# Kernel optimization log

Hardware: AMD Instinct MI355X
Metric: run time of the kernel (lower is better)

## Reference

```python
import jax, jax.numpy as jnp
import numpy as np

EPS = 1e-8


def setup_inputs() -> dict:
    key = jax.random.key(0)
    ks = jax.random.split(key, 10)
    B, Cin, H, W = 16, 256, 64, 64
    D, C = 128, 32
    return {
        "f_curr": jax.random.normal(ks[0], (B, Cin, H, W), jnp.float32),
        "mu_prior": jax.random.normal(ks[1], (B, D, C), jnp.float32),
        "log_sigma_prior": jax.random.normal(ks[2], (B, D, C), jnp.float32),
        "pi_prior": jax.random.uniform(ks[3], (B, C), jnp.float32),
        "mu_post": jax.random.normal(ks[4], (B, D), jnp.float32),
        "log_sigma_post": jax.random.normal(ks[5], (B, D), jnp.float32),
        "noise_cluster": jax.random.normal(ks[6], (B, D), jnp.float32),
        "noise_z": jax.random.normal(ks[7], (B, D), jnp.float32),
        "proj_W": jax.random.normal(ks[8], (Cin, Cin + D), jnp.float32) * 0.02,
        "proj_b": jax.random.normal(ks[9], (Cin,), jnp.float32) * 0.02,
    }


def reference(f_curr, mu_prior, log_sigma_prior, pi_prior, mu_post,
              log_sigma_post, noise_cluster, noise_z, proj_W, proj_b):
    sg = jax.lax.stop_gradient

    # ---- _cluster_sampler (all stats detached in the original) ----
    mu_p, ls_p = sg(mu_post), sg(log_sigma_post)          # [B, D]
    mu_pr, ls_pr = sg(mu_prior), sg(log_sigma_prior)      # [B, D, C]
    z_post = mu_p + jnp.exp(ls_p) * noise_cluster          # Normal(mu, exp(ls)).sample()
    sigma_pr = jnp.exp(ls_pr)
    # Normal log_prob of z_post[:, :, None] under each cluster -> [B, D, C]
    log_probs = (-ls_pr - 0.5 * jnp.log(2.0 * jnp.pi)
                 - (z_post[:, :, None] - mu_pr) ** 2 / (2.0 * sigma_pr ** 2))
    log_prob_c = jnp.sum(log_probs, axis=1)                # [B, C]
    pi_post = jax.nn.softmax(log_prob_c, axis=1)           # [B, C]

    # ---- z_c = Normal(mu_post, exp(ls)+eps).sample()  (no grad: .sample()) ----
    z_c = sg(mu_post + (jnp.exp(log_sigma_post) + EPS) * noise_z)  # [B, D]

    # ---- _f_combine: concat + 1x1 conv, computed as split matmuls ----
    Cin = f_curr.shape[1]
    Wf, Wz = proj_W[:, :Cin], proj_W[:, Cin:]              # [Cin,Cin], [Cin,D]
    bias = jnp.einsum('bd,od->bo', z_c, Wz) + proj_b       # spatially-constant part
    f_out = jnp.einsum('bchw,oc->bohw', f_curr, Wf) + bias[:, :, None, None]

    # ---- _kld ----
    mu_post_e = mu_post[:, :, None]                        # [B, D, 1]
    ls_post_e = log_sigma_post[:, :, None]
    sigma_prior = jnp.exp(log_sigma_prior)
    sigma_post = jnp.exp(ls_post_e)
    kl_g = (log_sigma_prior - ls_post_e
            + (sigma_post ** 2 + (mu_post_e - mu_prior) ** 2)
            / (2.0 * sigma_prior ** 2 + EPS) - 0.5)
    kl_g = jnp.sum(kl_g, axis=1)                           # [B, C]
    kl_g_weighted = jnp.sum(pi_post * kl_g, axis=1)        # [B]
    kl_cat = jnp.sum(pi_post * (jnp.log(pi_post + EPS) - jnp.log(pi_prior + EPS)), axis=1)  # [B]
    kl_std = jnp.sum(-ls_post_e + 0.5 * (jnp.exp(2.0 * ls_post_e) + mu_post_e ** 2) - 0.5,
                     axis=1)                               # [B, 1]
    # NOTE: original torch code broadcasts [B] + [B,1] -> [B,B] before mean; replicated here.
    kld = jnp.mean((kl_g_weighted + kl_cat) + kl_std)

    return f_out, kld
```

## Files before the change

kernel.cpp:

```cpp
#include <hip/hip_runtime.h>
#include <math.h>

#define EPS_F 1e-8f

typedef __attribute__((ext_vector_type(8))) short bf16x8;
typedef __attribute__((ext_vector_type(4))) float f32x4;

__device__ inline short f2bf(float f) {
    union { float f; unsigned u; } v; v.f = f;
    unsigned r = (v.u + 0x7fffu + ((v.u >> 16) & 1u)) >> 16;
    return (short)r;
}

__global__ __launch_bounds__(256) void prelim_kernel(
    const float* __restrict__ mu_prior,
    const float* __restrict__ ls_prior,
    const float* __restrict__ pi_prior,
    const float* __restrict__ mu_post,
    const float* __restrict__ ls_post,
    const float* __restrict__ noise_c,
    const float* __restrict__ noise_z,
    const float* __restrict__ projW,
    const float* __restrict__ projb,
    float* __restrict__ ws_bias,
    short* __restrict__ ws_A,
    float* __restrict__ kld_out)
{
    const int b = blockIdx.x;
    const int t = threadIdx.x;

    {
        const float* wrow = projW + t * 384 + b * 16;
        bf16x8 w0, w1;
#pragma unroll
        for (int j = 0; j < 8; ++j) w0[j] = f2bf(wrow[j]);
#pragma unroll
        for (int j = 0; j < 8; ++j) w1[j] = f2bf(wrow[8 + j]);
        *(bf16x8*)&ws_A[(b * 2 + 0) * 2048 + t * 8] = w0;
        *(bf16x8*)&ws_A[(b * 2 + 1) * 2048 + t * 8] = w1;
    }

    __shared__ float s_zpost[128];
    __shared__ float s_zc[128];
    __shared__ float s_mu[128];
    __shared__ float s_e2[128];
    __shared__ float s_lsp[128];
    __shared__ float s_kstd[128];
    __shared__ float s_p1[8][32];
    __shared__ float s_p2[8][32];

    if (t < 128) {
        const float mu = mu_post[b * 128 + t];
        const float ls = ls_post[b * 128 + t];
        const float el = __expf(ls);
        s_zpost[t] = mu + el * noise_c[b * 128 + t];
        s_zc[t]    = mu + (el + EPS_F) * noise_z[b * 128 + t];
        s_mu[t]    = mu;
        s_e2[t]    = el * el;
        s_lsp[t]   = ls;
        s_kstd[t]  = -ls + 0.5f * (el * el + mu * mu) - 0.5f;
    }
    __syncthreads();

    {
        const int c = t & 31;
        const int g = t >> 5;
        const float* mpB = mu_prior + b * 4096;
        const float* lpB = ls_prior + b * 4096;
        float lp = 0.f, kg = 0.f;
#pragma unroll 4
        for (int j = 0; j < 16; ++j) {
            const int d = g * 16 + j;
            const float mpr  = mpB[d * 32 + c];
            const float lpr  = lpB[d * 32 + c];
            const float inv2 = 0.5f * __expf(-2.f * lpr);
            const float zd   = s_zpost[d] - mpr;
            lp += -lpr - 0.91893853320467274f - zd * zd * inv2;
            const float dm   = s_mu[d] - mpr;
            const float e2pr = __expf(2.f * lpr);
            kg += lpr - s_lsp[d]
                + (s_e2[d] + dm * dm) * __builtin_amdgcn_rcpf(2.f * e2pr + EPS_F)
                - 0.5f;
        }
        s_p1[g][c] = lp;
        s_p2[g][c] = kg;
    }
    __syncthreads();

    if (t < 64) {
        const int c = t & 31;
        float lp = 0.f, kg = 0.f;
#pragma unroll
        for (int g = 0; g < 8; ++g) { lp += s_p1[g][c]; kg += s_p2[g][c]; }
        float ks = s_kstd[c] + s_kstd[c + 32] + s_kstd[c + 64] + s_kstd[c + 96];
        const float pp = pi_prior[b * 32 + c];

        float m = lp;
#pragma unroll
        for (int o = 16; o; o >>= 1) m = fmaxf(m, __shfl_xor(m, o, 32));
        const float e = __expf(lp - m);
        float den = e;
#pragma unroll
        for (int o = 16; o; o >>= 1) den += __shfl_xor(den, o, 32);
        const float pi = e * __builtin_amdgcn_rcpf(den);
        float tot = pi * kg + pi * (__logf(pi + EPS_F) - __logf(pp + EPS_F));
#pragma unroll
        for (int o = 16; o; o >>= 1) tot += __shfl_xor(tot, o, 32);
#pragma unroll
        for (int o = 16; o; o >>= 1) ks += __shfl_xor(ks, o, 32);
        if (t == 0) atomicAdd(kld_out, (tot + ks) * 0.0625f);
    }

    {
        const int o = t;
        const float4* wrow = (const float4*)(projW + o * 384 + 256);
        float sum = projb[o];
#pragma unroll 8
        for (int j = 0; j < 32; ++j) {
            const float4 w = wrow[j];
            sum += s_zc[4 * j + 0] * w.x + s_zc[4 * j + 1] * w.y +
                   s_zc[4 * j + 2] * w.z + s_zc[4 * j + 3] * w.w;
        }
        ws_bias[b * 256 + o] = sum;
    }
}

__global__ __launch_bounds__(256) void gemm_kernel(
    const float* __restrict__ F,
    const short* __restrict__ wsA,
    const float* __restrict__ bias,
    float* __restrict__ O)
{
    const int nT = blockIdx.x;
    const int oT = blockIdx.y;
    const int b  = blockIdx.z;

    __shared__ float s_bias[128];

    const int tid  = threadIdx.x;
    const int lane = tid & 63;
    const int wave = tid >> 6;
    const int wm = wave & 1;
    const int wn = wave >> 1;
    const int kg = lane >> 4;
    const int lm = lane & 15;

    if (tid < 128) s_bias[tid] = bias[b * 256 + oT * 128 + tid];

    const short* aBase = wsA + (size_t)kg * 2048 + (oT * 128 + wm * 64 + lm) * 8;
    const float* bBase = F + (size_t)b * 1048576 + (size_t)(kg * 8) * 4096
                       + nT * 128 + wn * 64 + lm;

    f32x4 acc[4][4];
#pragma unroll
    for (int i = 0; i < 4; ++i)
#pragma unroll
        for (int j = 0; j < 4; ++j) acc[i][j] = (f32x4){0.f, 0.f, 0.f, 0.f};

    float Bbuf[2][32];

#pragma unroll
    for (int nt = 0; nt < 4; ++nt)
#pragma unroll
        for (int j = 0; j < 8; ++j)
            Bbuf[0][nt * 8 + j] = bBase[(size_t)j * 4096 + nt * 16];

#pragma unroll
    for (int kc = 0; kc < 8; ++kc) {
        const int cur = kc & 1, nxt = cur ^ 1;

        if (kc < 7) {
            const float* bp = bBase + (size_t)(kc + 1) * 32 * 4096;
#pragma unroll
            for (int nt = 0; nt < 4; ++nt)
#pragma unroll
                for (int j = 0; j < 8; ++j)
                    Bbuf[nxt][nt * 8 + j] = bp[(size_t)j * 4096 + nt * 16];
        }

        bf16x8 aF[4];
#pragma unroll
        for (int mt = 0; mt < 4; ++mt)
            aF[mt] = *(const bf16x8*)(aBase + (size_t)kc * 8192 + mt * 128);

        bf16x8 bF[4];
#pragma unroll
        for (int nt = 0; nt < 4; ++nt)
#pragma unroll
            for (int j = 0; j < 8; ++j)
                bF[nt][j] = f2bf(Bbuf[cur][nt * 8 + j]);

#pragma unroll
        for (int mt = 0; mt < 4; ++mt)
#pragma unroll
            for (int nt = 0; nt < 4; ++nt)
                acc[mt][nt] = __builtin_amdgcn_mfma_f32_16x16x32_bf16(
                    aF[mt], bF[nt], acc[mt][nt], 0, 0, 0);
    }

    __syncthreads();

    float* Ob = O + (size_t)b * 1048576 + (size_t)oT * 128 * 4096;
    const int rbase = wm * 64 + kg * 4;
    const int cbase = nT * 128 + wn * 64 + lm;
#pragma unroll
    for (int mt = 0; mt < 4; ++mt) {
#pragma unroll
        for (int r = 0; r < 4; ++r) {
            const int row = rbase + mt * 16 + r;
            const float bb = s_bias[row];
            float* orow = Ob + (size_t)row * 4096 + cbase;
#pragma unroll
            for (int nt = 0; nt < 4; ++nt)
                orow[nt * 16] = acc[mt][nt][r] + bb;
        }
    }
}

extern "C" void kernel_launch(void* const* d_in, const int* in_sizes, int n_in,
                              void* d_out, int out_size, void* d_ws, size_t ws_size,
                              hipStream_t stream) {
    const float* f_curr   = (const float*)d_in[0];
    const float* mu_prior = (const float*)d_in[1];
    const float* ls_prior = (const float*)d_in[2];
    const float* pi_prior = (const float*)d_in[3];
    const float* mu_post  = (const float*)d_in[4];
    const float* ls_post  = (const float*)d_in[5];
    const float* noise_c  = (const float*)d_in[6];
    const float* noise_z  = (const float*)d_in[7];
    const float* projW    = (const float*)d_in[8];
    const float* projb    = (const float*)d_in[9];

    float* out = (float*)d_out;
    float* ws  = (float*)d_ws;
    float* ws_bias = ws;
    short* ws_A    = (short*)(ws + 4096);

    float* kld_out = out + 16777216;
    hipMemsetAsync(kld_out, 0, sizeof(float), stream);

    prelim_kernel<<<16, 256, 0, stream>>>(mu_prior, ls_prior, pi_prior, mu_post,
                                          ls_post, noise_c, noise_z, projW, projb,
                                          ws_bias, ws_A, kld_out);
    gemm_kernel<<<dim3(32, 2, 16), 256, 0, stream>>>(f_curr, ws_A, ws_bias, out);
}
```

Before: 164.7 us.

## Stage full-K bf16 F tile in LDS and cover all output channels per block

```diff
diff --git a/kernel.cpp b/kernel.cpp
--- a/kernel.cpp
+++ b/kernel.cpp
@@ -132,24 +132,46 @@
     float* __restrict__ O)
 {
     const int nT = blockIdx.x;
-    const int oT = blockIdx.y;
-    const int b  = blockIdx.z;
-
-    __shared__ float s_bias[128];
+    const int b  = blockIdx.y;
+
+    __shared__ short Bl[32][64][8];
+    __shared__ float s_bias[256];
 
     const int tid  = threadIdx.x;
     const int lane = tid & 63;
     const int wave = tid >> 6;
-    const int wm = wave & 1;
-    const int wn = wave >> 1;
-    const int kg = lane >> 4;
-    const int lm = lane & 15;
-
-    if (tid < 128) s_bias[tid] = bias[b * 256 + oT * 128 + tid];
-
-    const short* aBase = wsA + (size_t)kg * 2048 + (oT * 128 + wm * 64 + lm) * 8;
-    const float* bBase = F + (size_t)b * 1048576 + (size_t)(kg * 8) * 4096
-                       + nT * 128 + wn * 64 + lm;
+    const int kg   = lane >> 4;
+    const int lm   = lane & 15;
+
+    s_bias[tid] = bias[b * 256 + tid];
+
+    const int sn4 = (tid & 15) * 4;
+    const int skb = (tid >> 4) * 16;
+    const float* fp = F + (size_t)b * 1048576 + (size_t)skb * 4096
+                    + nT * 64 + sn4;
+
+    float4 ld[16];
+#pragma unroll
+    for (int i = 0; i < 16; ++i)
+        ld[i] = *(const float4*)(fp + (size_t)i * 4096);
+
+#pragma unroll
+    for (int h = 0; h < 2; ++h) {
+        const int kgi = (skb >> 3) + h;
+#pragma unroll
+        for (int c = 0; c < 4; ++c) {
+            bf16x8 v;
+#pragma unroll
+            for (int j = 0; j < 8; ++j) {
+                const float4 q = ld[h * 8 + j];
+                v[j] = f2bf(c == 0 ? q.x : c == 1 ? q.y : c == 2 ? q.z : q.w);
+            }
+            *(bf16x8*)&Bl[kgi][sn4 + c][0] = v;
+        }
+    }
+    __syncthreads();
+
+    const short* aBase = wsA + (size_t)kg * 2048 + (wave * 64 + lm) * 8;
 
     f32x4 acc[4][4];
 #pragma unroll
@@ -157,38 +179,15 @@
 #pragma unroll
         for (int j = 0; j < 4; ++j) acc[i][j] = (f32x4){0.f, 0.f, 0.f, 0.f};
 
-    float Bbuf[2][32];
-
-#pragma unroll
-    for (int nt = 0; nt < 4; ++nt)
-#pragma unroll
-        for (int j = 0; j < 8; ++j)
-            Bbuf[0][nt * 8 + j] = bBase[(size_t)j * 4096 + nt * 16];
-
 #pragma unroll
     for (int kc = 0; kc < 8; ++kc) {
-        const int cur = kc & 1, nxt = cur ^ 1;
-
-        if (kc < 7) {
-            const float* bp = bBase + (size_t)(kc + 1) * 32 * 4096;
-#pragma unroll
-            for (int nt = 0; nt < 4; ++nt)
-#pragma unroll
-                for (int j = 0; j < 8; ++j)
-                    Bbuf[nxt][nt * 8 + j] = bp[(size_t)j * 4096 + nt * 16];
-        }
-
-        bf16x8 aF[4];
+        bf16x8 aF[4], bF[4];
 #pragma unroll
         for (int mt = 0; mt < 4; ++mt)
             aF[mt] = *(const bf16x8*)(aBase + (size_t)kc * 8192 + mt * 128);
-
-        bf16x8 bF[4];
 #pragma unroll
         for (int nt = 0; nt < 4; ++nt)
-#pragma unroll
-            for (int j = 0; j < 8; ++j)
-                bF[nt][j] = f2bf(Bbuf[cur][nt * 8 + j]);
+            bF[nt] = *(const bf16x8*)&Bl[kc * 4 + kg][nt * 16 + lm][0];
 
 #pragma unroll
         for (int mt = 0; mt < 4; ++mt)
@@ -198,11 +197,9 @@
                     aF[mt], bF[nt], acc[mt][nt], 0, 0, 0);
     }
 
-    __syncthreads();
-
-    float* Ob = O + (size_t)b * 1048576 + (size_t)oT * 128 * 4096;
-    const int rbase = wm * 64 + kg * 4;
-    const int cbase = nT * 128 + wn * 64 + lm;
+    float* Ob = O + (size_t)b * 1048576 + nT * 64;
+    const int rbase = wave * 64 + kg * 4;
+    const int cbase = lm;
 #pragma unroll
     for (int mt = 0; mt < 4; ++mt) {
 #pragma unroll
@@ -242,5 +239,5 @@
     prelim_kernel<<<16, 256, 0, stream>>>(mu_prior, ls_prior, pi_prior, mu_post,
                                           ls_post, noise_c, noise_z, projW, projb,
                                           ws_bias, ws_A, kld_out);
-    gemm_kernel<<<dim3(32, 2, 16), 256, 0, stream>>>(f_curr, ws_A, ws_bias, out);
-}
+    gemm_kernel<<<dim3(64, 16), 256, 0, stream>>>(f_curr, ws_A, ws_bias, out);
+}
```

Measured after the change: 146.2 us. 11.2% less time.
